# Performance work log

Measured on AMD Instinct MI355X. Metric: run time of the kernel, lower is better.

## Reference

```python
import jax, jax.numpy as jnp
import numpy as np

B, T, F, D, K, C, O = 256, 16, 8, 32, 64, 1024, 2

def setup_inputs():
    ks = jax.random.split(jax.random.key(0), 16)
    return {
        "tdata": jax.random.normal(ks[0], (B, T, F, D), jnp.float32),
        "f_mask": jax.random.randint(ks[1], (B, T, F), 0, 2, jnp.int32),
        "centers": jax.random.normal(ks[2], (F, K, D), jnp.float32),
        "pat": jax.random.randint(ks[3], (F, C, F), 0, K + 2, jnp.int32),
        "pat_rep": jax.random.normal(ks[4], (F, C, D), jnp.float32),
        "pos_cnt": jax.random.uniform(ks[5], (F, C), jnp.float32),
        "neg_cnt": jax.random.uniform(ks[6], (F, C), jnp.float32),
        "W_q": jax.random.normal(ks[7], (F, D, D), jnp.float32) * 0.1,
        "b_q": jax.random.normal(ks[8], (F, D), jnp.float32) * 0.1,
        "W_k": jax.random.normal(ks[9], (F, D, D + 1), jnp.float32) * 0.1,
        "b_k": jax.random.normal(ks[10], (F, D), jnp.float32) * 0.1,
        "W_v": jax.random.normal(ks[11], (F, D + 1, D + 1), jnp.float32) * 0.1,
        "b_v": jax.random.normal(ks[12], (F, D + 1), jnp.float32) * 0.1,
        "W_pred": jax.random.normal(ks[13], (O, F * (D + 1)), jnp.float32) * 0.1,
    }

def reference(tdata, f_mask, centers, pat, pat_rep, pos_cnt, neg_cnt,
              W_q, b_q, W_k, b_k, W_v, b_v, W_pred):
    Bv, Tv, Fv, Dv = tdata.shape
    BT = Bv * Tv
    fdata = tdata.reshape(BT, Fv, Dv)                     # [BT, F, D]

    # --- VQ nearest-centroid codes per feature (compute_codes) ---
    def codes_one(x, cen):                                # x [BT, D], cen [K, D]
        d = (jnp.sum(x * x, 1, keepdims=True)
             - 2.0 * (x @ cen.T)
             + jnp.sum(cen * cen, 1)[None, :])
        return jnp.argmin(d, axis=1)
    codes = jax.vmap(codes_one, in_axes=(1, 0), out_axes=1)(fdata, centers)  # [BT, F]
    mflat = f_mask.reshape(BT, Fv)
    # scatter_add equivalent: masked positions get code+2, unmasked get 1
    f_codes = jnp.where(mflat != 0, codes.astype(jnp.int32) + 2, 1)          # [BT, F]

    ratio = pos_cnt / (pos_cnt + neg_cnt + 1e-6)          # [F, C]
    rep = jnp.concatenate([pat_rep, ratio[..., None]], axis=-1)  # [F, C, D+1]
    query = tdata[:, -1]                                  # [B, F, D]

    def per_feature(pat_i, rep_i, q_i, Wq, bq, Wk, bk, Wv, bv):
        # pattern match: wildcard (0) always matches, else code must equal
        wild = pat_i == 0                                 # [C, F]
        eq = jnp.where(wild[None], True, f_codes[:, None, :] == pat_i[None])  # [BT, C, F]
        match = jnp.any(jnp.all(eq, axis=2).reshape(Bv, Tv, -1), axis=1)      # [B, C]
        key_t = match[..., None].astype(rep_i.dtype) * rep_i[None]            # [B, C, D+1]
        iq = q_i @ Wq.T + bq                              # [B, D]
        ik = key_t @ Wk.T + bk                            # [B, C, D]
        iv = key_t @ Wv.T + bv                            # [B, C, D+1]
        e = jnp.einsum('bcd,bd->bc', ik, iq)
        e = e - (1.0 - match.astype(e.dtype)) * 1e7
        a = jax.nn.softmax(e, axis=-1)
        v = jnp.einsum('bc,bcd->bd', a, iv)               # [B, D+1]
        return v, a

    v_all, a_all = jax.vmap(per_feature, in_axes=(0, 0, 1, 0, 0, 0, 0, 0, 0))(
        pat, rep, query, W_q, b_q, W_k, b_k, W_v, b_v)    # [F,B,D+1], [F,B,C]
    srep = jnp.swapaxes(v_all, 0, 1)                      # [B, F, D+1]
    fm = jnp.any(f_mask != 0, axis=1).astype(srep.dtype)  # [B, F]
    srep = srep * fm[..., None]
    cali = srep.reshape(Bv, -1) @ W_pred.T                # [B, O]
    return cali, a_all, srep
```

## Files before the change

### kernel.cpp

```cpp
#include <hip/hip_runtime.h>
#include <math.h>

#define Bv 256
#define Tv 16
#define Fv 8
#define Dv 32
#define Kv 64
#define Cv 1024
#define Ov 2
#define D1 33

typedef unsigned long long u64;
typedef unsigned char u8;

__global__ __launch_bounds__(256) void k1(
    const float* __restrict__ tdata, const int* __restrict__ f_mask,
    const float* __restrict__ centers, const int* __restrict__ pat,
    u8* __restrict__ cbytes, u64* __restrict__ pat64, u64* __restrict__ care64,
    float* __restrict__ cali) {
  int blk = blockIdx.x, tid = threadIdx.x;
  if (blk < 128) {
    int ff = blk >> 4;
    int bt = ((blk & 15) << 8) + tid;
    __shared__ float ccs[Kv];
    if (tid < Kv) {
      const float* cr = centers + (ff * Kv + tid) * Dv;
      float s = 0.f;
      #pragma unroll
      for (int j = 0; j < Dv; j++) { float cv = cr[j]; s += cv * cv; }
      ccs[tid] = s;
    }
    const float4* xr = (const float4*)(tdata + (size_t)(bt * Fv + ff) * Dv);
    float4 xq[8];
    #pragma unroll
    for (int i = 0; i < 8; i++) xq[i] = xr[i];
    __syncthreads();
    float dmin = INFINITY; int kmin = 0;
    const float4* cb = (const float4*)(centers + ff * Kv * Dv);
    #pragma unroll 2
    for (int k = 0; k < Kv; k++) {
      const float4* cr = cb + k * 8;
      float4 dv = make_float4(0.f, 0.f, 0.f, 0.f);
      #pragma unroll
      for (int i = 0; i < 8; i++) {
        float4 cq = cr[i];
        dv.x += xq[i].x * cq.x; dv.y += xq[i].y * cq.y;
        dv.z += xq[i].z * cq.z; dv.w += xq[i].w * cq.w;
      }
      float dot = (dv.x + dv.y) + (dv.z + dv.w);
      float d = ccs[k] - 2.0f * dot;
      if (d < dmin) { dmin = d; kmin = k; }
    }
    int m = f_mask[bt * Fv + ff];
    cbytes[bt * Fv + ff] = (u8)(m != 0 ? kmin + 2 : 1);
  } else if (blk < 160) {
    int fc = ((blk - 128) << 8) + tid;
    const int* pr = pat + fc * Fv;
    u64 pp = 0, cm = 0;
    #pragma unroll
    for (int ff = 0; ff < Fv; ff++) {
      int pv = pr[ff];
      pp |= ((u64)(pv & 0xFF)) << (8 * ff);
      if (pv != 0) cm |= 0xFFull << (8 * ff);
    }
    pat64[fc] = pp;
    care64[fc] = cm;
  } else {
    cali[tid] = 0.f;
    cali[tid + 256] = 0.f;
  }
}

__global__ __launch_bounds__(256) void k2(
    const float* __restrict__ tdata, const int* __restrict__ f_mask,
    const float* __restrict__ W_q, const float* __restrict__ b_q,
    const float* __restrict__ W_k, const float* __restrict__ b_k,
    const float* __restrict__ W_v, const float* __restrict__ b_v,
    const float* __restrict__ W_pred,
    const float* __restrict__ pat_rep, const float* __restrict__ pos_cnt,
    const float* __restrict__ neg_cnt,
    const u64* __restrict__ code64, const u64* __restrict__ pat64,
    const u64* __restrict__ care64,
    float* __restrict__ a_out, float* __restrict__ srep_out,
    float* __restrict__ cali) {
  int b = blockIdx.x, f = blockIdx.y, tid = threadIdx.x;
  __shared__ u64 cds[Tv];
  __shared__ int fmv[Tv];
  __shared__ int fm_sh;
  __shared__ int anyf[4];
  __shared__ float vsum[D1];
  __shared__ float qs[Dv], iqs[Dv], zs[D1 + 1];
  __shared__ float redm[4], reds[4];

  if (tid < Tv) cds[tid] = code64[b * Tv + tid];
  if (tid >= 32 && tid < 32 + Tv) fmv[tid - 32] = f_mask[(b * Tv + (tid - 32)) * Fv + f];
  if (tid < D1) vsum[tid] = 0.f;
  if (tid >= 60 && tid < 64) anyf[tid - 60] = 0;
  __syncthreads();
  if (tid == 0) {
    int a = 0;
    #pragma unroll
    for (int t = 0; t < Tv; t++) a |= fmv[t];
    fm_sh = (a != 0);
  }

  int c0 = tid * 4;
  const u64* p64 = pat64 + f * Cv;
  const u64* c64 = care64 + f * Cv;
  u64 pp[4], cm[4];
  #pragma unroll
  for (int j = 0; j < 4; j++) { pp[j] = p64[c0 + j]; cm[j] = c64[c0 + j]; }
  bool mt[4];
  #pragma unroll
  for (int j = 0; j < 4; j++) {
    bool m = false;
    #pragma unroll
    for (int t = 0; t < Tv; t++) m = m || (((cds[t] ^ pp[j]) & cm[j]) == 0ull);
    mt[j] = m;
  }
  bool lany = mt[0] || mt[1] || mt[2] || mt[3];
  if (__any((int)lany) && (tid & 63) == 0) anyf[tid >> 6] = 1;
  __syncthreads();
  bool anym = (anyf[0] | anyf[1] | anyf[2] | anyf[3]) != 0;

  float4* arow = (float4*)(a_out + (size_t)(f * Bv + b) * Cv);

  if (!anym) {
    const float u = 1.0f / 1024.0f;
    arow[tid] = make_float4(u, u, u, u);
    if (tid < D1) {
      float vd = fm_sh ? b_v[f * D1 + tid] : 0.f;
      srep_out[(b * Fv + f) * D1 + tid] = vd;
      vsum[tid] = vd;
    }
    __syncthreads();
    if (tid < Ov) {
      const float* w = W_pred + tid * (Fv * D1) + f * D1;
      float acc = 0.f;
      #pragma unroll
      for (int j = 0; j < D1; j++) acc += vsum[j] * w[j];
      atomicAdd(&cali[b * Ov + tid], acc);
    }
    return;
  }

  if (tid < Dv) qs[tid] = tdata[((b * Tv + (Tv - 1)) * Fv + f) * Dv + tid];
  __syncthreads();
  if (tid < Dv) {
    const float* w = W_q + (f * Dv + tid) * Dv;
    float s = b_q[f * Dv + tid];
    #pragma unroll
    for (int j = 0; j < Dv; j++) s += w[j] * qs[j];
    iqs[tid] = s;
  }
  __syncthreads();
  if (tid < D1) {
    float s = 0.f;
    #pragma unroll
    for (int i = 0; i < Dv; i++) s += W_k[(f * Dv + i) * D1 + tid] * iqs[i];
    zs[tid] = s;
  }
  if (tid == D1) {
    float s = 0.f;
    #pragma unroll
    for (int i = 0; i < Dv; i++) s += b_k[f * Dv + i] * iqs[i];
    zs[D1] = s;
  }
  __syncthreads();

  float ev[4];
  float lmax = -INFINITY;
  #pragma unroll
  for (int j = 0; j < 4; j++) {
    ev[j] = 0.f;
    if (mt[j]) {
      int c = c0 + j;
      const float* rp = pat_rep + (size_t)(f * Cv + c) * Dv;
      float p = pos_cnt[f * Cv + c], n = neg_cnt[f * Cv + c];
      float r = p / (p + n + 1e-6f);
      float s = zs[D1] + r * zs[Dv];
      for (int jj = 0; jj < Dv; jj++) s += rp[jj] * zs[jj];
      ev[j] = s;
      lmax = fmaxf(lmax, s);
    }
  }
  float mx = lmax;
  #pragma unroll
  for (int off = 32; off >= 1; off >>= 1) mx = fmaxf(mx, __shfl_xor(mx, off, 64));
  if ((tid & 63) == 0) redm[tid >> 6] = mx;
  __syncthreads();
  float bmax = fmaxf(fmaxf(redm[0], redm[1]), fmaxf(redm[2], redm[3]));

  float av[4] = {0.f, 0.f, 0.f, 0.f};
  float ls = 0.f;
  #pragma unroll
  for (int j = 0; j < 4; j++) {
    if (mt[j]) { av[j] = expf(ev[j] - bmax); ls += av[j]; }
  }
  float ss = ls;
  #pragma unroll
  for (int off = 32; off >= 1; off >>= 1) ss += __shfl_xor(ss, off, 64);
  if ((tid & 63) == 0) reds[tid >> 6] = ss;
  __syncthreads();
  float Z = reds[0] + reds[1] + reds[2] + reds[3];

  float4 aq = make_float4(av[0] / Z, av[1] / Z, av[2] / Z, av[3] / Z);
  arow[tid] = aq;

  #pragma unroll
  for (int j = 0; j < 4; j++) {
    if (mt[j] && av[j] != 0.f) {
      float a = av[j] / Z;
      int c = c0 + j;
      const float* rp = pat_rep + (size_t)(f * Cv + c) * Dv;
      float p = pos_cnt[f * Cv + c], n = neg_cnt[f * Cv + c];
      float r = p / (p + n + 1e-6f);
      for (int jj = 0; jj < Dv; jj++) atomicAdd(&vsum[jj], a * rp[jj]);
      atomicAdd(&vsum[Dv], a * r);
    }
  }
  __syncthreads();
  float vreg = 0.f;
  if (tid < D1) {
    float s = b_v[f * D1 + tid];
    const float* w = W_v + (f * D1 + tid) * D1;
    for (int j = 0; j < D1; j++) s += w[j] * vsum[j];
    vreg = s;
  }
  __syncthreads();
  if (tid < D1) {
    float vd = fm_sh ? vreg : 0.f;
    srep_out[(b * Fv + f) * D1 + tid] = vd;
    vsum[tid] = vd;
  }
  __syncthreads();
  if (tid < Ov) {
    const float* w = W_pred + tid * (Fv * D1) + f * D1;
    float acc = 0.f;
    #pragma unroll
    for (int j = 0; j < D1; j++) acc += vsum[j] * w[j];
    atomicAdd(&cali[b * Ov + tid], acc);
  }
}

extern "C" void kernel_launch(void* const* d_in, const int* in_sizes, int n_in,
                              void* d_out, int out_size, void* d_ws, size_t ws_size,
                              hipStream_t stream) {
  const float* tdata   = (const float*)d_in[0];
  const int*   f_mask  = (const int*)d_in[1];
  const float* centers = (const float*)d_in[2];
  const int*   pat     = (const int*)d_in[3];
  const float* pat_rep = (const float*)d_in[4];
  const float* pos_cnt = (const float*)d_in[5];
  const float* neg_cnt = (const float*)d_in[6];
  const float* W_q     = (const float*)d_in[7];
  const float* b_q     = (const float*)d_in[8];
  const float* W_k     = (const float*)d_in[9];
  const float* b_k     = (const float*)d_in[10];
  const float* W_v     = (const float*)d_in[11];
  const float* b_v     = (const float*)d_in[12];
  const float* W_pred  = (const float*)d_in[13];

  float* out = (float*)d_out;
  float* cali = out;
  float* a_all = out + (Bv * Ov);
  float* srep = out + (Bv * Ov) + (Fv * (size_t)Bv * Cv);

  char* ws = (char*)d_ws;
  u8*  cbytes = (u8*)(ws);
  u64* code64 = (u64*)(ws);
  u64* pat64  = (u64*)(ws + 32768);
  u64* care64 = (u64*)(ws + 98304);

  k1<<<161, 256, 0, stream>>>(tdata, f_mask, centers, pat,
                              cbytes, pat64, care64, cali);
  k2<<<dim3(Bv, Fv), 256, 0, stream>>>(tdata, f_mask, W_q, b_q, W_k, b_k,
                                       W_v, b_v, W_pred,
                                       pat_rep, pos_cnt, neg_cnt,
                                       code64, pat64, care64,
                                       a_all, srep, cali);
}
```

Measured before the change: 107.1 us.

## Fuse code computation and attention into a single kernel with redundant recompute

Merges the two kernels into one launch. Each (b,f) block recomputes VQ codes for its batch row and builds pattern masks inline from raw pat, so the workspace round-trip and the inter-kernel dependency go away. An extra set of 256 blocks recomputes all eight features per batch row to produce cali without atomics. This removes one launch and the cali zeroing, at the cost of 8x redundant nearest-centroid work per block and serial per-feature attention in the extra cali blocks, which may form a long tail.

```diff
diff --git a/kernel.cpp b/kernel.cpp
--- a/kernel.cpp
+++ b/kernel.cpp
@@ -13,158 +13,150 @@
 typedef unsigned long long u64;
 typedef unsigned char u8;
 
-__global__ __launch_bounds__(256) void k1(
-    const float* __restrict__ tdata, const int* __restrict__ f_mask,
-    const float* __restrict__ centers, const int* __restrict__ pat,
-    u8* __restrict__ cbytes, u64* __restrict__ pat64, u64* __restrict__ care64,
-    float* __restrict__ cali) {
-  int blk = blockIdx.x, tid = threadIdx.x;
-  if (blk < 128) {
-    int ff = blk >> 4;
-    int bt = ((blk & 15) << 8) + tid;
-    __shared__ float ccs[Kv];
-    if (tid < Kv) {
-      const float* cr = centers + (ff * Kv + tid) * Dv;
-      float s = 0.f;
-      #pragma unroll
-      for (int j = 0; j < Dv; j++) { float cv = cr[j]; s += cv * cv; }
-      ccs[tid] = s;
-    }
-    const float4* xr = (const float4*)(tdata + (size_t)(bt * Fv + ff) * Dv);
-    float4 xq[8];
-    #pragma unroll
-    for (int i = 0; i < 8; i++) xq[i] = xr[i];
-    __syncthreads();
-    float dmin = INFINITY; int kmin = 0;
-    const float4* cb = (const float4*)(centers + ff * Kv * Dv);
-    #pragma unroll 2
-    for (int k = 0; k < Kv; k++) {
-      const float4* cr = cb + k * 8;
-      float4 dv = make_float4(0.f, 0.f, 0.f, 0.f);
-      #pragma unroll
-      for (int i = 0; i < 8; i++) {
-        float4 cq = cr[i];
-        dv.x += xq[i].x * cq.x; dv.y += xq[i].y * cq.y;
-        dv.z += xq[i].z * cq.z; dv.w += xq[i].w * cq.w;
-      }
-      float dot = (dv.x + dv.y) + (dv.z + dv.w);
-      float d = ccs[k] - 2.0f * dot;
-      if (d < dmin) { dmin = d; kmin = k; }
-    }
+struct SM {
+  float ccs[Fv * Kv];
+  u64   cds[Tv];
+  float srep_all[Fv * D1];
+  float vsum[D1];
+  float qs[Dv], iqs[Dv], zs[D1 + 1];
+  float redm[4], reds[4];
+  int   fm_arr[Fv];
+  int   fm_any;
+  int   anyf[4];
+};
+
+__device__ __forceinline__ void compute_codes(
+    SM& sm, int b, const float* __restrict__ tdata,
+    const int* __restrict__ f_mask, const float* __restrict__ centers) {
+  int tid = threadIdx.x;
+  #pragma unroll
+  for (int r = 0; r < 2; r++) {
+    int idx = tid + r * 256;
+    const float* cr = centers + idx * Dv;
+    float s = 0.f;
+    #pragma unroll
+    for (int j = 0; j < Dv; j++) { float cv = cr[j]; s += cv * cv; }
+    sm.ccs[idx] = s;
+  }
+  int pair = tid >> 1, half = tid & 1;
+  int t = pair >> 3, ff = pair & 7;
+  int bt = b * Tv + t;
+  const float4* xr = (const float4*)(tdata + (size_t)(bt * Fv + ff) * Dv);
+  float4 xq[8];
+  #pragma unroll
+  for (int i = 0; i < 8; i++) xq[i] = xr[i];
+  __syncthreads();
+  int k0 = half * 32;
+  const float4* cb = (const float4*)(centers + (size_t)(ff * Kv + k0) * Dv);
+  float dmin = INFINITY; int kmin = k0;
+  for (int k = 0; k < 32; k++) {
+    const float4* cr = cb + k * 8;
+    float4 dv = make_float4(0.f, 0.f, 0.f, 0.f);
+    #pragma unroll
+    for (int i = 0; i < 8; i++) {
+      float4 cq = cr[i];
+      dv.x += xq[i].x * cq.x; dv.y += xq[i].y * cq.y;
+      dv.z += xq[i].z * cq.z; dv.w += xq[i].w * cq.w;
+    }
+    float dot = (dv.x + dv.y) + (dv.z + dv.w);
+    float d = sm.ccs[ff * Kv + k0 + k] - 2.0f * dot;
+    if (d < dmin) { dmin = d; kmin = k0 + k; }
+  }
+  float od = __shfl_xor(dmin, 1, 64);
+  int ok = __shfl_xor(kmin, 1, 64);
+  if (od < dmin || (od == dmin && ok < kmin)) { dmin = od; kmin = ok; }
+  if (half == 0) {
     int m = f_mask[bt * Fv + ff];
-    cbytes[bt * Fv + ff] = (u8)(m != 0 ? kmin + 2 : 1);
-  } else if (blk < 160) {
-    int fc = ((blk - 128) << 8) + tid;
-    const int* pr = pat + fc * Fv;
-    u64 pp = 0, cm = 0;
-    #pragma unroll
-    for (int ff = 0; ff < Fv; ff++) {
-      int pv = pr[ff];
-      pp |= ((u64)(pv & 0xFF)) << (8 * ff);
-      if (pv != 0) cm |= 0xFFull << (8 * ff);
-    }
-    pat64[fc] = pp;
-    care64[fc] = cm;
-  } else {
-    cali[tid] = 0.f;
-    cali[tid + 256] = 0.f;
-  }
+    ((u8*)sm.cds)[t * Fv + ff] = (u8)(m != 0 ? kmin + 2 : 1);
+  }
+  __syncthreads();
 }
 
-__global__ __launch_bounds__(256) void k2(
-    const float* __restrict__ tdata, const int* __restrict__ f_mask,
+__device__ __forceinline__ void attn_feature(
+    SM& sm, int b, int f, bool write_out, const int* fm_flag,
+    const float* __restrict__ tdata,
+    const int* __restrict__ pat, const float* __restrict__ pat_rep,
+    const float* __restrict__ pos_cnt, const float* __restrict__ neg_cnt,
     const float* __restrict__ W_q, const float* __restrict__ b_q,
     const float* __restrict__ W_k, const float* __restrict__ b_k,
     const float* __restrict__ W_v, const float* __restrict__ b_v,
-    const float* __restrict__ W_pred,
-    const float* __restrict__ pat_rep, const float* __restrict__ pos_cnt,
-    const float* __restrict__ neg_cnt,
-    const u64* __restrict__ code64, const u64* __restrict__ pat64,
-    const u64* __restrict__ care64,
-    float* __restrict__ a_out, float* __restrict__ srep_out,
-    float* __restrict__ cali) {
-  int b = blockIdx.x, f = blockIdx.y, tid = threadIdx.x;
-  __shared__ u64 cds[Tv];
-  __shared__ int fmv[Tv];
-  __shared__ int fm_sh;
-  __shared__ int anyf[4];
-  __shared__ float vsum[D1];
-  __shared__ float qs[Dv], iqs[Dv], zs[D1 + 1];
-  __shared__ float redm[4], reds[4];
-
-  if (tid < Tv) cds[tid] = code64[b * Tv + tid];
-  if (tid >= 32 && tid < 32 + Tv) fmv[tid - 32] = f_mask[(b * Tv + (tid - 32)) * Fv + f];
-  if (tid < D1) vsum[tid] = 0.f;
-  if (tid >= 60 && tid < 64) anyf[tid - 60] = 0;
-  __syncthreads();
-  if (tid == 0) {
-    int a = 0;
-    #pragma unroll
-    for (int t = 0; t < Tv; t++) a |= fmv[t];
-    fm_sh = (a != 0);
-  }
+    float* __restrict__ a_out, float* __restrict__ srep_out) {
+  int tid = threadIdx.x;
+  if (tid < 4) sm.anyf[tid] = 0;
+
+  u64 creg[Tv];
+  #pragma unroll
+  for (int t = 0; t < Tv; t++) creg[t] = sm.cds[t];
 
   int c0 = tid * 4;
-  const u64* p64 = pat64 + f * Cv;
-  const u64* c64 = care64 + f * Cv;
+  const int* pbase = pat + ((size_t)f * Cv + c0) * Fv;
   u64 pp[4], cm[4];
   #pragma unroll
-  for (int j = 0; j < 4; j++) { pp[j] = p64[c0 + j]; cm[j] = c64[c0 + j]; }
+  for (int j = 0; j < 4; j++) {
+    int4 pa = ((const int4*)(pbase + j * Fv))[0];
+    int4 pb = ((const int4*)(pbase + j * Fv))[1];
+    int vals[8] = {pa.x, pa.y, pa.z, pa.w, pb.x, pb.y, pb.z, pb.w};
+    u64 P = 0, M = 0;
+    #pragma unroll
+    for (int ff = 0; ff < Fv; ff++) {
+      P |= ((u64)(vals[ff] & 0xFF)) << (8 * ff);
+      if (vals[ff] != 0) M |= 0xFFull << (8 * ff);
+    }
+    pp[j] = P; cm[j] = M;
+  }
   bool mt[4];
   #pragma unroll
   for (int j = 0; j < 4; j++) {
     bool m = false;
     #pragma unroll
-    for (int t = 0; t < Tv; t++) m = m || (((cds[t] ^ pp[j]) & cm[j]) == 0ull);
+    for (int t = 0; t < Tv; t++) m = m || (((creg[t] ^ pp[j]) & cm[j]) == 0ull);
     mt[j] = m;
   }
   bool lany = mt[0] || mt[1] || mt[2] || mt[3];
-  if (__any((int)lany) && (tid & 63) == 0) anyf[tid >> 6] = 1;
-  __syncthreads();
-  bool anym = (anyf[0] | anyf[1] | anyf[2] | anyf[3]) != 0;
+  __syncthreads();
+  bool wv = __any((int)lany);
+  if ((tid & 63) == 0) sm.anyf[tid >> 6] = wv ? 1 : 0;
+  __syncthreads();
+  bool anym = (sm.anyf[0] | sm.anyf[1] | sm.anyf[2] | sm.anyf[3]) != 0;
+  bool fm = (*fm_flag) != 0;
 
   float4* arow = (float4*)(a_out + (size_t)(f * Bv + b) * Cv);
 
   if (!anym) {
-    const float u = 1.0f / 1024.0f;
-    arow[tid] = make_float4(u, u, u, u);
+    if (write_out) {
+      const float u = 1.0f / 1024.0f;
+      arow[tid] = make_float4(u, u, u, u);
+    }
     if (tid < D1) {
-      float vd = fm_sh ? b_v[f * D1 + tid] : 0.f;
-      srep_out[(b * Fv + f) * D1 + tid] = vd;
-      vsum[tid] = vd;
-    }
-    __syncthreads();
-    if (tid < Ov) {
-      const float* w = W_pred + tid * (Fv * D1) + f * D1;
-      float acc = 0.f;
-      #pragma unroll
-      for (int j = 0; j < D1; j++) acc += vsum[j] * w[j];
-      atomicAdd(&cali[b * Ov + tid], acc);
+      float vd = fm ? b_v[f * D1 + tid] : 0.f;
+      sm.vsum[tid] = vd;
+      if (write_out) srep_out[(b * Fv + f) * D1 + tid] = vd;
     }
     return;
   }
 
-  if (tid < Dv) qs[tid] = tdata[((b * Tv + (Tv - 1)) * Fv + f) * Dv + tid];
+  if (tid < D1) sm.vsum[tid] = 0.f;
+  if (tid < Dv) sm.qs[tid] = tdata[((b * Tv + (Tv - 1)) * Fv + f) * Dv + tid];
   __syncthreads();
   if (tid < Dv) {
     const float* w = W_q + (f * Dv + tid) * Dv;
     float s = b_q[f * Dv + tid];
     #pragma unroll
-    for (int j = 0; j < Dv; j++) s += w[j] * qs[j];
-    iqs[tid] = s;
+    for (int j = 0; j < Dv; j++) s += w[j] * sm.qs[j];
+    sm.iqs[tid] = s;
   }
   __syncthreads();
   if (tid < D1) {
     float s = 0.f;
     #pragma unroll
-    for (int i = 0; i < Dv; i++) s += W_k[(f * Dv + i) * D1 + tid] * iqs[i];
-    zs[tid] = s;
+    for (int i = 0; i < Dv; i++) s += W_k[(f * Dv + i) * D1 + tid] * sm.iqs[i];
+    sm.zs[tid] = s;
   }
   if (tid == D1) {
     float s = 0.f;
     #pragma unroll
-    for (int i = 0; i < Dv; i++) s += b_k[f * Dv + i] * iqs[i];
-    zs[D1] = s;
+    for (int i = 0; i < Dv; i++) s += b_k[f * Dv + i] * sm.iqs[i];
+    sm.zs[D1] = s;
   }
   __syncthreads();
 
@@ -178,8 +170,8 @@
       const float* rp = pat_rep + (size_t)(f * Cv + c) * Dv;
       float p = pos_cnt[f * Cv + c], n = neg_cnt[f * Cv + c];
       float r = p / (p + n + 1e-6f);
-      float s = zs[D1] + r * zs[Dv];
-      for (int jj = 0; jj < Dv; jj++) s += rp[jj] * zs[jj];
+      float s = sm.zs[D1] + r * sm.zs[Dv];
+      for (int jj = 0; jj < Dv; jj++) s += rp[jj] * sm.zs[jj];
       ev[j] = s;
       lmax = fmaxf(lmax, s);
     }
@@ -187,9 +179,9 @@
   float mx = lmax;
   #pragma unroll
   for (int off = 32; off >= 1; off >>= 1) mx = fmaxf(mx, __shfl_xor(mx, off, 64));
-  if ((tid & 63) == 0) redm[tid >> 6] = mx;
-  __syncthreads();
-  float bmax = fmaxf(fmaxf(redm[0], redm[1]), fmaxf(redm[2], redm[3]));
+  if ((tid & 63) == 0) sm.redm[tid >> 6] = mx;
+  __syncthreads();
+  float bmax = fmaxf(fmaxf(sm.redm[0], sm.redm[1]), fmaxf(sm.redm[2], sm.redm[3]));
 
   float av[4] = {0.f, 0.f, 0.f, 0.f};
   float ls = 0.f;
@@ -200,12 +192,11 @@
   float ss = ls;
   #pragma unroll
   for (int off = 32; off >= 1; off >>= 1) ss += __shfl_xor(ss, off, 64);
-  if ((tid & 63) == 0) reds[tid >> 6] = ss;
-  __syncthreads();
-  float Z = reds[0] + reds[1] + reds[2] + reds[3];
-
-  float4 aq = make_float4(av[0] / Z, av[1] / Z, av[2] / Z, av[3] / Z);
-  arow[tid] = aq;
+  if ((tid & 63) == 0) sm.reds[tid >> 6] = ss;
+  __syncthreads();
+  float Z = sm.reds[0] + sm.reds[1] + sm.reds[2] + sm.reds[3];
+
+  if (write_out) arow[tid] = make_float4(av[0] / Z, av[1] / Z, av[2] / Z, av[3] / Z);
 
   #pragma unroll
   for (int j = 0; j < 4; j++) {
@@ -215,8 +206,8 @@
       const float* rp = pat_rep + (size_t)(f * Cv + c) * Dv;
       float p = pos_cnt[f * Cv + c], n = neg_cnt[f * Cv + c];
       float r = p / (p + n + 1e-6f);
-      for (int jj = 0; jj < Dv; jj++) atomicAdd(&vsum[jj], a * rp[jj]);
-      atomicAdd(&vsum[Dv], a * r);
+      for (int jj = 0; jj < Dv; jj++) atomicAdd(&sm.vsum[jj], a * rp[jj]);
+      atomicAdd(&sm.vsum[Dv], a * r);
     }
   }
   __syncthreads();
@@ -224,22 +215,64 @@
   if (tid < D1) {
     float s = b_v[f * D1 + tid];
     const float* w = W_v + (f * D1 + tid) * D1;
-    for (int j = 0; j < D1; j++) s += w[j] * vsum[j];
+    for (int j = 0; j < D1; j++) s += w[j] * sm.vsum[j];
     vreg = s;
   }
   __syncthreads();
   if (tid < D1) {
-    float vd = fm_sh ? vreg : 0.f;
-    srep_out[(b * Fv + f) * D1 + tid] = vd;
-    vsum[tid] = vd;
-  }
-  __syncthreads();
-  if (tid < Ov) {
-    const float* w = W_pred + tid * (Fv * D1) + f * D1;
-    float acc = 0.f;
-    #pragma unroll
-    for (int j = 0; j < D1; j++) acc += vsum[j] * w[j];
-    atomicAdd(&cali[b * Ov + tid], acc);
+    float vd = fm ? vreg : 0.f;
+    sm.vsum[tid] = vd;
+    if (write_out) srep_out[(b * Fv + f) * D1 + tid] = vd;
+  }
+}
+
+__global__ __launch_bounds__(256) void fused(
+    const float* __restrict__ tdata, const int* __restrict__ f_mask,
+    const float* __restrict__ centers, const int* __restrict__ pat,
+    const float* __restrict__ pat_rep, const float* __restrict__ pos_cnt,
+    const float* __restrict__ neg_cnt,
+    const float* __restrict__ W_q, const float* __restrict__ b_q,
+    const float* __restrict__ W_k, const float* __restrict__ b_k,
+    const float* __restrict__ W_v, const float* __restrict__ b_v,
+    const float* __restrict__ W_pred,
+    float* __restrict__ cali, float* __restrict__ a_out,
+    float* __restrict__ srep_out) {
+  __shared__ SM sm;
+  int blk = blockIdx.x, tid = threadIdx.x;
+
+  if (blk < Fv * Bv) {
+    int f = blk >> 8, b = blk & 255;
+    compute_codes(sm, b, tdata, f_mask, centers);
+    int mloc = (tid < Tv) ? f_mask[(b * Tv + tid) * Fv + f] : 0;
+    bool fmw = __any(mloc != 0);
+    if (tid == 0) sm.fm_any = fmw ? 1 : 0;
+    attn_feature(sm, b, f, true, &sm.fm_any, tdata, pat, pat_rep,
+                 pos_cnt, neg_cnt, W_q, b_q, W_k, b_k, W_v, b_v,
+                 a_out, srep_out);
+  } else {
+    int b = blk - Fv * Bv;
+    compute_codes(sm, b, tdata, f_mask, centers);
+    if (tid < Fv) sm.fm_arr[tid] = 0;
+    __syncthreads();
+    if (tid < Tv * Fv) {
+      int t = tid >> 3, ffi = tid & 7;
+      if (f_mask[(b * Tv + t) * Fv + ffi] != 0) sm.fm_arr[ffi] = 1;
+    }
+    for (int f = 0; f < Fv; f++) {
+      attn_feature(sm, b, f, false, &sm.fm_arr[f], tdata, pat, pat_rep,
+                   pos_cnt, neg_cnt, W_q, b_q, W_k, b_k, W_v, b_v,
+                   a_out, srep_out);
+      __syncthreads();
+      if (tid < D1) sm.srep_all[f * D1 + tid] = sm.vsum[tid];
+      __syncthreads();
+    }
+    if (tid < Ov) {
+      const float* w = W_pred + tid * (Fv * D1);
+      float acc = 0.f;
+      #pragma unroll 8
+      for (int i = 0; i < Fv * D1; i++) acc += sm.srep_all[i] * w[i];
+      cali[b * Ov + tid] = acc;
+    }
   }
 }
 
@@ -266,17 +299,8 @@
   float* a_all = out + (Bv * Ov);
   float* srep = out + (Bv * Ov) + (Fv * (size_t)Bv * Cv);
 
-  char* ws = (char*)d_ws;
-  u8*  cbytes = (u8*)(ws);
-  u64* code64 = (u64*)(ws);
-  u64* pat64  = (u64*)(ws + 32768);
-  u64* care64 = (u64*)(ws + 98304);
-
-  k1<<<161, 256, 0, stream>>>(tdata, f_mask, centers, pat,
-                              cbytes, pat64, care64, cali);
-  k2<<<dim3(Bv, Fv), 256, 0, stream>>>(tdata, f_mask, W_q, b_q, W_k, b_k,
-                                       W_v, b_v, W_pred,
-                                       pat_rep, pos_cnt, neg_cnt,
-                                       code64, pat64, care64,
-                                       a_all, srep, cali);
+  fused<<<Fv * Bv + Bv, 256, 0, stream>>>(
+      tdata, f_mask, centers, pat, pat_rep, pos_cnt, neg_cnt,
+      W_q, b_q, W_k, b_k, W_v, b_v, W_pred,
+      cali, a_all, srep);
 }
```

New measurement: 386.1 us. +260.6%, slower.
